# Kernel tuning notes

Measured on AMD Instinct MI355X. Metric: run time of the kernel, lower is better.

Reference implementation:

```python
import jax, jax.numpy as jnp
import numpy as np

G = 4            # group order (e.g., C4)
H = 16           # attention heads
DH = 64          # head dim
D = 1024         # token dim = H*DH = C*G
DI = 4096        # FFN inner dim
MAXREL = 32      # relative position clamp
EPS = 1e-5


def eq_ln(x):
    # Equivariant LayerNorm: (N, D) -> (N, G, D/G), LN over last dim, no affine
    N, Dt = x.shape
    xr = x.reshape(N, G, Dt // G)
    mu = jnp.mean(xr, axis=-1, keepdims=True)
    var = jnp.var(xr, axis=-1, keepdims=True)
    return ((xr - mu) * jax.lax.rsqrt(var + EPS)).reshape(N, Dt)


def ada_ln(x, temb, w, b):
    # AdaLN: scale/shift from SiLU(temb) -> Linear -> chunk
    n = eq_ln(x)
    ss = jax.nn.silu(temb) @ w.T + b                      # (N, 2D)
    scale, shift = jnp.split(ss, 2, axis=1)
    return n * (1.0 + scale) + shift


def attention(xq, xkv, wq, wk, wv, wo, bo, rel_table):
    # xq: (B,Tq,D), xkv: (B,Tk,D); rel_table: (H, 2*MAXREL+1) or None
    B, Tq, _ = xq.shape
    Tk = xkv.shape[1]
    q = (xq @ wq.T).reshape(B, Tq, H, DH)
    k = (xkv @ wk.T).reshape(B, Tk, H, DH)
    v = (xkv @ wv.T).reshape(B, Tk, H, DH)
    scores = jnp.einsum('bthd,bkhd->bhtk', q, k) * (DH ** -0.5)
    if rel_table is not None:
        rel_idx = jnp.clip(jnp.arange(Tq)[:, None] - jnp.arange(Tk)[None, :],
                           -MAXREL, MAXREL) + MAXREL      # (Tq, Tk)
        scores = scores + rel_table[:, rel_idx][None]     # (1,H,Tq,Tk)
    attn = jax.nn.softmax(scores, axis=-1)
    out = jnp.einsum('bhtk,bkhd->bthd', attn, v).reshape(B, Tq, H * DH)
    return out @ wo.T + bo


def setup_inputs() -> dict:
    key = jax.random.key(0)
    ks = jax.random.split(key, 24)
    s = 0.02
    B, T = 4, 1024
    inp = {
        'hidden_states': jax.random.normal(ks[0], (B, T, D), jnp.float32),
        'encoder_hidden_states': jax.random.normal(ks[1], (B, T, D), jnp.float32),
        'temb': jax.random.normal(ks[2], (B * T, D), jnp.float32),
        # AdaLN 1 / 2
        'w_ada1': jax.random.normal(ks[3], (2 * D, D), jnp.float32) * s,
        'b_ada1': jnp.zeros((2 * D,), jnp.float32),
        'w_ada2': jax.random.normal(ks[4], (2 * D, D), jnp.float32) * s,
        'b_ada2': jnp.zeros((2 * D,), jnp.float32),
        # self-attention (attention_bias=False, out_bias=True)
        'wq1': jax.random.normal(ks[5], (D, D), jnp.float32) * s,
        'wk1': jax.random.normal(ks[6], (D, D), jnp.float32) * s,
        'wv1': jax.random.normal(ks[7], (D, D), jnp.float32) * s,
        'wo1': jax.random.normal(ks[8], (D, D), jnp.float32) * s,
        'bo1': jnp.zeros((D,), jnp.float32),
        'rel_bias': jax.random.normal(ks[9], (H, 2 * MAXREL + 1), jnp.float32) * s,
        # cross-attention
        'wq2': jax.random.normal(ks[10], (D, D), jnp.float32) * s,
        'wk2': jax.random.normal(ks[11], (D, D), jnp.float32) * s,
        'wv2': jax.random.normal(ks[12], (D, D), jnp.float32) * s,
        'wo2': jax.random.normal(ks[13], (D, D), jnp.float32) * s,
        'bo2': jnp.zeros((D,), jnp.float32),
        # GEGLU FFN
        'w_ff1': jax.random.normal(ks[14], (2 * DI, D), jnp.float32) * s,
        'b_ff1': jnp.zeros((2 * DI,), jnp.float32),
        'w_ff2': jax.random.normal(ks[15], (D, DI), jnp.float32) * s,
        'b_ff2': jnp.zeros((D,), jnp.float32),
    }
    return inp


def reference(hidden_states, encoder_hidden_states, temb,
              w_ada1, b_ada1, w_ada2, b_ada2,
              wq1, wk1, wv1, wo1, bo1, rel_bias,
              wq2, wk2, wv2, wo2, bo2,
              w_ff1, b_ff1, w_ff2, b_ff2):
    B, T, Dm = hidden_states.shape
    x = hidden_states.reshape(B * T, Dm)
    # 1) AdaLN + self-attention with relative position bias + residual
    x1 = ada_ln(x, temb, w_ada1, b_ada1).reshape(B, T, Dm)
    x = x + attention(x1, x1, wq1, wk1, wv1, wo1, bo1, rel_bias).reshape(B * T, Dm)
    # 2) AdaLN + cross-attention + residual
    x2 = ada_ln(x, temb, w_ada2, b_ada2).reshape(B, T, Dm)
    x = x + attention(x2, encoder_hidden_states, wq2, wk2, wv2, wo2, bo2,
                      None).reshape(B * T, Dm)
    # 3) LayerNorm + GEGLU FFN + residual
    n3 = eq_ln(x)
    h12 = n3 @ w_ff1.T + b_ff1                            # (N, 2*DI)
    a, g = jnp.split(h12, 2, axis=-1)
    ff = (a * jax.nn.gelu(g, approximate=False)) @ w_ff2.T + b_ff2
    x = x + ff
    return x.reshape(B, T, Dm)
```

## Files before the change

kernel.cpp:

```cpp
#include <hip/hip_runtime.h>
#include <math.h>

typedef __attribute__((ext_vector_type(4))) float f32x4;
typedef __attribute__((ext_vector_type(8))) __bf16 bf16x8;

#define MFMA_BF16(a, b, c) __builtin_amdgcn_mfma_f32_16x16x32_bf16((a), (b), (c), 0, 0, 0)

static __device__ __forceinline__ unsigned short f2b(float f) {
  unsigned int u = __float_as_uint(f);
  return (unsigned short)((u + 0x7FFFu + ((u >> 16) & 1u)) >> 16);
}
static __device__ __forceinline__ float b2f(unsigned short h) {
  return __uint_as_float(((unsigned int)h) << 16);
}
static __device__ __forceinline__ unsigned short bcvt(float f) {
  __bf16 h = (__bf16)f;
  return __builtin_bit_cast(unsigned short, h);
}

static __device__ __forceinline__ void gll16(const void* g, void* l) {
  __builtin_amdgcn_global_load_lds((const __attribute__((address_space(1))) void*)g,
                                   (__attribute__((address_space(3))) void*)l, 16, 0, 0);
}

struct CvtArgs {
  const float* src[12];
  unsigned short* dst[12];
  int start[12];
};
__global__ __launch_bounds__(256) void f2b_multi(CvtArgs a) {
  const int bid = blockIdx.x;
  int s = 11;
#pragma unroll
  for (int i = 11; i >= 1; --i)
    if (bid < a.start[i]) s = i - 1;
  const size_t i4 = (size_t)(bid - a.start[s]) * 256 + threadIdx.x;
  const float4 v = *(const float4*)(a.src[s] + i4 * 4);
  ushort4 o;
  o.x = f2b(v.x); o.y = f2b(v.y); o.z = f2b(v.z); o.w = f2b(v.w);
  *(ushort4*)(a.dst[s] + i4 * 4) = o;
}

__global__ __launch_bounds__(256) void f2bperm_kernel(const float* __restrict__ src,
                                                      unsigned short* __restrict__ dst) {
  const int r = blockIdx.x;
  const int rr = r & 4095;
  const int dr = ((rr >> 4) << 5) | ((r >> 12) << 4) | (rr & 15);
  const int c = threadIdx.x * 4;
  const float4 v = *(const float4*)(src + (size_t)r * 1024 + c);
  ushort4 o;
  o.x = f2b(v.x); o.y = f2b(v.y); o.z = f2b(v.z); o.w = f2b(v.w);
  *(ushort4*)(dst + (size_t)dr * 1024 + c) = o;
}

__global__ __launch_bounds__(256) void silu_kernel(const float* __restrict__ src,
                                                   unsigned short* __restrict__ dst, int n) {
  const int i = (blockIdx.x * 256 + threadIdx.x) * 4;
  if (i >= n) return;
  const float4 v = *(const float4*)(src + i);
  ushort4 o;
  o.x = f2b(v.x / (1.f + expf(-v.x)));
  o.y = f2b(v.y / (1.f + expf(-v.y)));
  o.z = f2b(v.z / (1.f + expf(-v.z)));
  o.w = f2b(v.w / (1.f + expf(-v.w)));
  *(ushort4*)(dst + i) = o;
}

template <int ADA>
__global__ __launch_bounds__(256) void eqln_kernel(const float* __restrict__ x,
                                                   const unsigned short* __restrict__ ss,
                                                   unsigned short* __restrict__ outp) {
  const int n = blockIdx.x;
  const int tid = threadIdx.x;
  const int g = tid >> 6, lane = tid & 63;
  const size_t base = (size_t)n * 1024 + g * 256 + lane * 4;
  const float4 v = *(const float4*)(x + base);
  float s = v.x + v.y + v.z + v.w;
  float s2 = v.x * v.x + v.y * v.y + v.z * v.z + v.w * v.w;
#pragma unroll
  for (int m = 1; m < 64; m <<= 1) {
    s += __shfl_xor(s, m, 64);
    s2 += __shfl_xor(s2, m, 64);
  }
  const float mu = s * (1.f / 256.f);
  const float var = s2 * (1.f / 256.f) - mu * mu;
  const float rs = rsqrtf(var + 1e-5f);
  float o0 = (v.x - mu) * rs, o1 = (v.y - mu) * rs, o2 = (v.z - mu) * rs, o3 = (v.w - mu) * rs;
  if (ADA) {
    const size_t sb = (size_t)n * 4096 + g * 256 + lane * 4;
    const ushort4 scv = *(const ushort4*)(ss + sb);
    const ushort4 shv = *(const ushort4*)(ss + sb + 1024);
    o0 = o0 * (1.f + b2f(scv.x)) + b2f(shv.x);
    o1 = o1 * (1.f + b2f(scv.y)) + b2f(shv.y);
    o2 = o2 * (1.f + b2f(scv.z)) + b2f(shv.z);
    o3 = o3 * (1.f + b2f(scv.w)) + b2f(shv.w);
  }
  ushort4 ov;
  ov.x = f2b(o0); ov.y = f2b(o1); ov.z = f2b(o2); ov.w = f2b(o3);
  *(ushort4*)(outp + base) = ov;
}

__global__ __launch_bounds__(256) void vtrans_kernel(const unsigned short* __restrict__ v,
                                                     unsigned short* __restrict__ vt, int T,
                                                     int ld) {
  const int t0 = blockIdx.x * 64, h = blockIdx.y, b = blockIdx.z;
  __shared__ unsigned short tile[64][65];
  const int tid = threadIdx.x;
#pragma unroll
  for (int rr = 0; rr < 2; ++rr) {
    const int tok = rr * 32 + (tid >> 3);
    const int d8 = (tid & 7) * 8;
    const uint4 x = *(const uint4*)(v + (size_t)(b * T + t0 + tok) * ld + h * 64 + d8);
    const unsigned int* xs = (const unsigned int*)&x;
#pragma unroll
    for (int j = 0; j < 4; ++j) {
      tile[d8 + 2 * j][tok] = (unsigned short)(xs[j] & 0xffffu);
      tile[d8 + 2 * j + 1][tok] = (unsigned short)(xs[j] >> 16);
    }
  }
  __syncthreads();
#pragma unroll
  for (int rr = 0; rr < 2; ++rr) {
    const int d = rr * 32 + (tid >> 3);
    const int t8 = (tid & 7) * 8;
    uint4 ov;
    unsigned int* ou = (unsigned int*)&ov;
#pragma unroll
    for (int j = 0; j < 4; ++j)
      ou[j] = (unsigned int)tile[d][t8 + 2 * j] | ((unsigned int)tile[d][t8 + 2 * j + 1] << 16);
    *(uint4*)(vt + ((size_t)((b * 16 + h) * 64 + d)) * T + t0 + t8) = ov;
  }
}

template <int BM, int BIAS, int RES, int OUTMODE>
__global__ __launch_bounds__(256, 4) void gemm_nt(const unsigned short* __restrict__ A,
                                                  const unsigned short* __restrict__ Bw,
                                                  const float* __restrict__ bias,
                                                  const float* res, void* Cout,
                                                  int M, int N, int K) {
  constexpr int MB = BM / 32;
  __shared__ unsigned short As[BM * 64];
  __shared__ unsigned short Bs[128 * 64];
  const int m0 = blockIdx.x * BM, n0 = blockIdx.y * 128;
  const int tid = threadIdx.x, lane = tid & 63;
  const int wr = (tid >> 7) & 1, wc = (tid >> 6) & 1;
  const int lr = lane & 15, ls = lane >> 4;

  const f32x4 fz = {0.f, 0.f, 0.f, 0.f};
  f32x4 acc[MB][4];
#pragma unroll
  for (int m = 0; m < MB; ++m)
#pragma unroll
    for (int n = 0; n < 4; ++n) acc[m][n] = fz;

  for (int k0 = 0; k0 < K; k0 += 64) {
#pragma unroll
    for (int it = 0; it < BM / 32; ++it) {
      const int u = it * 256 + tid;
      const int row = u >> 3, gs = (u & 7) ^ (row & 7);
      gll16(A + (size_t)(m0 + row) * K + k0 + gs * 8, As + u * 8);
    }
#pragma unroll
    for (int it = 0; it < 4; ++it) {
      const int u = it * 256 + tid;
      const int row = u >> 3, gs = (u & 7) ^ (row & 7);
      gll16(Bw + (size_t)(n0 + row) * K + k0 + gs * 8, Bs + u * 8);
    }
    __syncthreads();
#pragma unroll
    for (int kk = 0; kk < 2; ++kk) {
      bf16x8 af[MB], bfr[4];
#pragma unroll
      for (int m = 0; m < MB; ++m) {
        const int row = wr * (BM / 2) + m * 16 + lr;
        const int slot = (kk * 4 + ls) ^ (row & 7);
        af[m] = *(const bf16x8*)(As + row * 64 + slot * 8);
      }
#pragma unroll
      for (int n = 0; n < 4; ++n) {
        const int col = wc * 64 + n * 16 + lr;
        const int slot = (kk * 4 + ls) ^ (col & 7);
        bfr[n] = *(const bf16x8*)(Bs + col * 64 + slot * 8);
      }
#pragma unroll
      for (int m = 0; m < MB; ++m)
#pragma unroll
        for (int n = 0; n < 4; ++n) acc[m][n] = MFMA_BF16(af[m], bfr[n], acc[m][n]);
    }
    __syncthreads();
  }

  if (OUTMODE == 2) {
    const int pn0 = n0 + wc * 64;
#pragma unroll
    for (int m = 0; m < MB; ++m) {
#pragma unroll
      for (int j = 0; j < 2; ++j) {
        const int ocol = (pn0 >> 1) + j * 16 + lr;
        const float ba = bias[ocol];
        const float bg = bias[(N >> 1) + ocol];
#pragma unroll
        for (int r = 0; r < 4; ++r) {
          const int row = m0 + wr * (BM / 2) + m * 16 + ls * 4 + r;
          const float a = acc[m][2 * j][r] + ba;
          const float g = acc[m][2 * j + 1][r] + bg;
          const float gl = 0.5f * g * (1.f + erff(g * 0.70710678118654752f));
          ((unsigned short*)Cout)[(size_t)row * (N >> 1) + ocol] = f2b(a * gl);
        }
      }
    }
    return;
  }
#pragma unroll
  for (int m = 0; m < MB; ++m) {
#pragma unroll
    for (int n = 0; n < 4; ++n) {
      const int col = n0 + wc * 64 + n * 16 + lr;
      float bv = 0.f;
      if (BIAS) bv = bias[col];
#pragma unroll
      for (int r = 0; r < 4; ++r) {
        const int row = m0 + wr * (BM / 2) + m * 16 + ls * 4 + r;
        float v = acc[m][n][r] + bv;
        if (RES) v += res[(size_t)row * N + col];
        if (OUTMODE == 1)
          ((unsigned short*)Cout)[(size_t)row * N + col] = f2b(v);
        else
          ((float*)Cout)[(size_t)row * N + col] = v;
      }
    }
  }
}

template <int RELB>
__global__ __launch_bounds__(256) void attn_kernel(const unsigned short* __restrict__ q,
                                                   const unsigned short* __restrict__ k,
                                                   const unsigned short* __restrict__ vt,
                                                   const float* __restrict__ rel,
                                                   unsigned short* __restrict__ outp,
                                                   int ldq, int ldk) {
  const int lin = blockIdx.x + (blockIdx.y << 4) + (blockIdx.z << 8);
  const int xcd = lin & 7, s = lin >> 3;
  const int g = (xcd << 3) + (s >> 4);
  const int qb = s & 15;
  const int h = g & 15, b = g >> 4;
  const int tid = threadIdx.x;
  const int wid = tid >> 6, lane = tid & 63;
  const int lr = lane & 15, ls = lane >> 4;
  const int q0 = (qb << 6) + (wid << 4);
  const float L2E = 1.44269504088896340736f;

  __shared__ unsigned short Ks[2][128 * 64];
  __shared__ unsigned short Vs[2][64 * 128];
  __shared__ unsigned short plds[4][16][64];
  __shared__ float tbl[66];

  if (RELB && tid < 65) tbl[tid] = rel[h * 65 + tid] * L2E;

  bf16x8 qa0, qa1;
  {
    const unsigned short* qp = q + (size_t)(b * 1024 + q0 + lr) * ldq + h * 64 + ls * 8;
    const bf16x8 t0 = *(const bf16x8*)qp;
    const bf16x8 t1 = *(const bf16x8*)(qp + 32);
    const float sc = 0.125f * L2E;
#pragma unroll
    for (int j = 0; j < 8; ++j) {
      qa0[j] = (__bf16)((float)t0[j] * sc);
      qa1[j] = (__bf16)((float)t1[j] * sc);
    }
  }
  bf16x8 ones;
#pragma unroll
  for (int j = 0; j < 8; ++j) ones[j] = (__bf16)1.0f;

  const f32x4 fz = {0.f, 0.f, 0.f, 0.f};
  f32x4 oacc[4];
#pragma unroll
  for (int d = 0; d < 4; ++d) oacc[d] = fz;
  f32x4 lacc = fz;

  const unsigned short* kbp = k + (size_t)(b * 1024) * ldk + h * 64;
  const unsigned short* vbp = vt + (size_t)((b * 16 + h) * 64) * 1024;

  auto stageK = [&](int buf, int kv0) {
#pragma unroll
    for (int it = 0; it < 4; ++it) {
      const int u = it * 256 + tid;
      const int row = u >> 3, gs = (u & 7) ^ (row & 7);
      gll16(kbp + (size_t)(kv0 + row) * ldk + gs * 8, Ks[buf] + u * 8);
    }
  };
  auto stageV = [&](int buf, int kv0) {
#pragma unroll
    for (int it = 0; it < 4; ++it) {
      const int u = it * 256 + tid;
      const int row = u >> 4;
      const int ch = u & 15;
      const int gs = (ch & 8) | ((ch & 7) ^ (row & 7));
      gll16(vbp + (size_t)row * 1024 + kv0 + gs * 8, Vs[buf] + u * 8);
    }
  };

  stageK(0, 0);
  stageV(0, 0);
  __syncthreads();

  for (int t = 0; t < 8; ++t) {
    const int kv0 = t << 7;
    if (t + 1 < 8) {
      stageV((t + 1) & 1, kv0 + 128);
      stageK((t + 1) & 1, kv0 + 128);
    }
    const unsigned short* kbuf = Ks[t & 1];
    const unsigned short* vbuf = Vs[t & 1];
#pragma unroll
    for (int sub = 0; sub < 2; ++sub) {
      const int kvs = kv0 + sub * 64;
      f32x4 sc4[4];
      __builtin_amdgcn_s_setprio(1);
#pragma unroll
      for (int nn = 0; nn < 4; ++nn) {
        const int row = sub * 64 + nn * 16 + lr;
        const int s0 = ls ^ (row & 7), s1 = (4 + ls) ^ (row & 7);
        const bf16x8 kb0 = *(const bf16x8*)(kbuf + row * 64 + s0 * 8);
        const bf16x8 kb1 = *(const bf16x8*)(kbuf + row * 64 + s1 * 8);
        f32x4 acc = fz;
        acc = MFMA_BF16(qa0, kb0, acc);
        acc = MFMA_BF16(qa1, kb1, acc);
        sc4[nn] = acc;
      }
      __builtin_amdgcn_s_setprio(0);
      float cb = 0.f;
      bool vary = false;
      if (RELB) {
        if (kvs + 95 <= q0) {
          cb = tbl[64];
        } else if (kvs >= q0 + 47) {
          cb = tbl[0];
        } else {
          vary = true;
        }
      }
      if (vary) {
        const int bd = q0 + ls * 4 - (kvs + lr);
#pragma unroll
        for (int nn = 0; nn < 4; ++nn)
#pragma unroll
          for (int r = 0; r < 4; ++r) {
            int dl = bd + r - nn * 16;
            dl = dl < -32 ? -32 : (dl > 32 ? 32 : dl);
            const float p = __builtin_amdgcn_exp2f(fminf(sc4[nn][r] + tbl[dl + 32], 60.f));
            const int qq = ls * 4 + r;
            const int colw = ((((nn << 1) + (lr >> 3)) ^ (qq & 7)) << 3) + (lr & 7);
            plds[wid][qq][colw] = bcvt(p);
          }
      } else {
#pragma unroll
        for (int nn = 0; nn < 4; ++nn)
#pragma unroll
          for (int r = 0; r < 4; ++r) {
            const float p = __builtin_amdgcn_exp2f(fminf(sc4[nn][r] + cb, 60.f));
            const int qq = ls * 4 + r;
            const int colw = ((((nn << 1) + (lr >> 3)) ^ (qq & 7)) << 3) + (lr & 7);
            plds[wid][qq][colw] = bcvt(p);
          }
      }
      asm volatile("" ::: "memory");
      const bf16x8 pa0 = *(const bf16x8*)&plds[wid][lr][((ls ^ (lr & 7)) << 3)];
      const bf16x8 pa1 = *(const bf16x8*)&plds[wid][lr][(((4 + ls) ^ (lr & 7)) << 3)];
      __builtin_amdgcn_s_setprio(1);
      lacc = MFMA_BF16(pa0, ones, lacc);
      lacc = MFMA_BF16(pa1, ones, lacc);
#pragma unroll
      for (int d = 0; d < 4; ++d) {
        const int rr = d * 16 + lr;
        const int c0 = sub * 8 + ls;
        const int c1 = c0 + 4;
        const int c0s = (c0 & 8) | ((c0 & 7) ^ (rr & 7));
        const int c1s = (c1 & 8) | ((c1 & 7) ^ (rr & 7));
        const bf16x8 vb0 = *(const bf16x8*)(vbuf + rr * 128 + c0s * 8);
        const bf16x8 vb1 = *(const bf16x8*)(vbuf + rr * 128 + c1s * 8);
        oacc[d] = MFMA_BF16(pa0, vb0, oacc[d]);
        oacc[d] = MFMA_BF16(pa1, vb1, oacc[d]);
      }
      __builtin_amdgcn_s_setprio(0);
    }
    __syncthreads();
  }

  float rinv[4];
#pragma unroll
  for (int r = 0; r < 4; ++r) rinv[r] = 1.0f / lacc[r];
#pragma unroll
  for (int d = 0; d < 4; ++d)
#pragma unroll
    for (int r = 0; r < 4; ++r) {
      const float v = oacc[d][r] * rinv[r];
      outp[(size_t)(b * 1024 + q0 + ls * 4 + r) * 1024 + h * 64 + d * 16 + lr] = bcvt(v);
    }
}

extern "C" void kernel_launch(void* const* d_in, const int* in_sizes, int n_in,
                              void* d_out, int out_size, void* d_ws, size_t ws_size,
                              hipStream_t stream) {
  (void)in_sizes; (void)n_in; (void)out_size; (void)ws_size;
  const float* hs = (const float*)d_in[0];
  const float* enc = (const float*)d_in[1];
  const float* temb = (const float*)d_in[2];
  const float* wada1 = (const float*)d_in[3];
  const float* bada1 = (const float*)d_in[4];
  const float* wada2 = (const float*)d_in[5];
  const float* bada2 = (const float*)d_in[6];
  const float* wq1 = (const float*)d_in[7];
  const float* wk1 = (const float*)d_in[8];
  const float* wv1 = (const float*)d_in[9];
  const float* wo1 = (const float*)d_in[10];
  const float* bo1 = (const float*)d_in[11];
  const float* rel = (const float*)d_in[12];
  const float* wq2 = (const float*)d_in[13];
  const float* wk2 = (const float*)d_in[14];
  const float* wv2 = (const float*)d_in[15];
  const float* wo2 = (const float*)d_in[16];
  const float* bo2 = (const float*)d_in[17];
  const float* wff1 = (const float*)d_in[18];
  const float* bff1 = (const float*)d_in[19];
  const float* wff2 = (const float*)d_in[20];
  const float* bff2 = (const float*)d_in[21];
  float* out = (float*)d_out;

  char* ws = (char*)d_ws;
  const size_t MB = 1024ull * 1024ull;
  unsigned short* wb_ada = (unsigned short*)(ws + 0 * MB);
  unsigned short* wb_q1 = (unsigned short*)(ws + 8 * MB);
  unsigned short* wb_k1 = (unsigned short*)(ws + 10 * MB);
  unsigned short* wb_v1 = (unsigned short*)(ws + 12 * MB);
  unsigned short* wb_o1 = (unsigned short*)(ws + 14 * MB);
  unsigned short* wb_q2 = (unsigned short*)(ws + 16 * MB);
  unsigned short* wb_k2 = (unsigned short*)(ws + 18 * MB);
  unsigned short* wb_v2 = (unsigned short*)(ws + 20 * MB);
  unsigned short* wb_o2 = (unsigned short*)(ws + 22 * MB);
  unsigned short* wb_ff1 = (unsigned short*)(ws + 24 * MB);
  unsigned short* wb_ff2 = (unsigned short*)(ws + 40 * MB);
  unsigned short* silu_t = (unsigned short*)(ws + 48 * MB);
  unsigned short* enc_b = (unsigned short*)(ws + 56 * MB);
  unsigned short* ssb = (unsigned short*)(ws + 64 * MB);
  unsigned short* ffin = (unsigned short*)(ws + 64 * MB);
  float* bias_cat = (float*)(ws + 96 * MB);
  unsigned short* x1b = (unsigned short*)(ws + 97 * MB);
  unsigned short* qkvb = (unsigned short*)(ws + 105 * MB);
  unsigned short* qb = (unsigned short*)(ws + 105 * MB);
  unsigned short* kvb = (unsigned short*)(ws + 113 * MB);
  unsigned short* vtb = (unsigned short*)(ws + 129 * MB);
  unsigned short* aob = (unsigned short*)(ws + 137 * MB);

  const int Nrow = 4096;

  {
    CvtArgs a;
    const float* srcs[12] = {wada1, wada2, wq1, wk1, wv1, wo1, wq2, wk2, wv2, wo2, wff2, enc};
    unsigned short* dsts[12] = {wb_ada, wb_ada + 2048 * 1024, wb_q1, wb_k1, wb_v1, wb_o1,
                                wb_q2, wb_k2, wb_v2, wb_o2, wb_ff2, enc_b};
    const int blks[12] = {2048, 2048, 1024, 1024, 1024, 1024, 1024, 1024, 1024, 1024, 4096, 4096};
    int acc = 0;
    for (int i = 0; i < 12; ++i) { a.src[i] = srcs[i]; a.dst[i] = dsts[i]; a.start[i] = acc; acc += blks[i]; }
    f2b_multi<<<acc, 256, 0, stream>>>(a);
  }
  (void)hipMemcpyAsync(bias_cat, bada1, 2048 * sizeof(float), hipMemcpyDeviceToDevice, stream);
  (void)hipMemcpyAsync(bias_cat + 2048, bada2, 2048 * sizeof(float), hipMemcpyDeviceToDevice, stream);
  f2bperm_kernel<<<8192, 256, 0, stream>>>(wff1, wb_ff1);
  silu_kernel<<<4096, 256, 0, stream>>>(temb, silu_t, 4096 * 1024);

  gemm_nt<128, 1, 0, 1><<<dim3(32, 32), 256, 0, stream>>>(silu_t, wb_ada, bias_cat, nullptr, ssb, Nrow, 4096, 1024);

  eqln_kernel<1><<<4096, 256, 0, stream>>>(hs, ssb, x1b);
  gemm_nt<128, 0, 0, 1><<<dim3(32, 24), 256, 0, stream>>>(x1b, wb_q1, nullptr, nullptr, qkvb, Nrow, 3072, 1024);
  vtrans_kernel<<<dim3(16, 16, 4), 256, 0, stream>>>(qkvb + 2048, vtb, 1024, 3072);
  attn_kernel<1><<<dim3(16, 16, 4), 256, 0, stream>>>(qkvb, qkvb + 1024, vtb, rel, aob, 3072, 3072);
  gemm_nt<64, 1, 1, 0><<<dim3(64, 8), 256, 0, stream>>>(aob, wb_o1, bo1, hs, out, Nrow, 1024, 1024);

  eqln_kernel<1><<<4096, 256, 0, stream>>>(out, ssb + 2048, x1b);
  gemm_nt<64, 0, 0, 1><<<dim3(64, 8), 256, 0, stream>>>(x1b, wb_q2, nullptr, nullptr, qb, Nrow, 1024, 1024);
  gemm_nt<128, 0, 0, 1><<<dim3(32, 16), 256, 0, stream>>>(enc_b, wb_k2, nullptr, nullptr, kvb, Nrow, 2048, 1024);
  vtrans_kernel<<<dim3(16, 16, 4), 256, 0, stream>>>(kvb + 1024, vtb, 1024, 2048);
  attn_kernel<0><<<dim3(16, 16, 4), 256, 0, stream>>>(qb, kvb, vtb, nullptr, aob, 1024, 2048);
  gemm_nt<64, 1, 1, 0><<<dim3(64, 8), 256, 0, stream>>>(aob, wb_o2, bo2, out, out, Nrow, 1024, 1024);

  eqln_kernel<0><<<4096, 256, 0, stream>>>(out, nullptr, x1b);
  gemm_nt<128, 1, 0, 2><<<dim3(32, 64), 256, 0, stream>>>(x1b, wb_ff1, bff1, nullptr, ffin, Nrow, 8192, 1024);
  gemm_nt<64, 1, 1, 0><<<dim3(64, 8), 256, 0, stream>>>(ffin, wb_ff2, bff2, out, out, Nrow, 1024, 4096);
}
```

Before: 428.3 us.

## Shrink attention KV tiles to single-buffered 64-row tiles to cut LDS use

The attention kernel drops its double-buffered 128-row K/V shared-memory tiles and uses one 64-row K and V tile per iteration. The next tile is loaded only after the current one is consumed. This cuts LDS from about 66KB to about 18KB, so more blocks can fit on each CU. In exchange, load/compute overlap inside a block is lost and there are twice as many iterations and barriers.

```diff
diff --git a/kernel.cpp b/kernel.cpp
--- a/kernel.cpp
+++ b/kernel.cpp
@@ -250,8 +250,8 @@
   const int q0 = (qb << 6) + (wid << 4);
   const float L2E = 1.44269504088896340736f;
 
-  __shared__ unsigned short Ks[2][128 * 64];
-  __shared__ unsigned short Vs[2][64 * 128];
+  __shared__ unsigned short Ks[64 * 64];
+  __shared__ unsigned short Vs[64 * 64];
   __shared__ unsigned short plds[4][16][64];
   __shared__ float tbl[66];
 
@@ -282,110 +282,101 @@
   const unsigned short* kbp = k + (size_t)(b * 1024) * ldk + h * 64;
   const unsigned short* vbp = vt + (size_t)((b * 16 + h) * 64) * 1024;
 
-  auto stageK = [&](int buf, int kv0) {
-#pragma unroll
-    for (int it = 0; it < 4; ++it) {
+  auto stageK = [&](int kv0) {
+#pragma unroll
+    for (int it = 0; it < 2; ++it) {
       const int u = it * 256 + tid;
       const int row = u >> 3, gs = (u & 7) ^ (row & 7);
-      gll16(kbp + (size_t)(kv0 + row) * ldk + gs * 8, Ks[buf] + u * 8);
+      gll16(kbp + (size_t)(kv0 + row) * ldk + gs * 8, Ks + u * 8);
     }
   };
-  auto stageV = [&](int buf, int kv0) {
-#pragma unroll
-    for (int it = 0; it < 4; ++it) {
+  auto stageV = [&](int kv0) {
+#pragma unroll
+    for (int it = 0; it < 2; ++it) {
       const int u = it * 256 + tid;
-      const int row = u >> 4;
-      const int ch = u & 15;
-      const int gs = (ch & 8) | ((ch & 7) ^ (row & 7));
-      gll16(vbp + (size_t)row * 1024 + kv0 + gs * 8, Vs[buf] + u * 8);
+      const int row = u >> 3, ch = u & 7;
+      const int gs = ch ^ (row & 7);
+      gll16(vbp + (size_t)row * 1024 + kv0 + gs * 8, Vs + u * 8);
     }
   };
 
-  stageK(0, 0);
-  stageV(0, 0);
-  __syncthreads();
-
-  for (int t = 0; t < 8; ++t) {
-    const int kv0 = t << 7;
-    if (t + 1 < 8) {
-      stageV((t + 1) & 1, kv0 + 128);
-      stageK((t + 1) & 1, kv0 + 128);
-    }
-    const unsigned short* kbuf = Ks[t & 1];
-    const unsigned short* vbuf = Vs[t & 1];
-#pragma unroll
-    for (int sub = 0; sub < 2; ++sub) {
-      const int kvs = kv0 + sub * 64;
-      f32x4 sc4[4];
-      __builtin_amdgcn_s_setprio(1);
-#pragma unroll
-      for (int nn = 0; nn < 4; ++nn) {
-        const int row = sub * 64 + nn * 16 + lr;
-        const int s0 = ls ^ (row & 7), s1 = (4 + ls) ^ (row & 7);
-        const bf16x8 kb0 = *(const bf16x8*)(kbuf + row * 64 + s0 * 8);
-        const bf16x8 kb1 = *(const bf16x8*)(kbuf + row * 64 + s1 * 8);
-        f32x4 acc = fz;
-        acc = MFMA_BF16(qa0, kb0, acc);
-        acc = MFMA_BF16(qa1, kb1, acc);
-        sc4[nn] = acc;
+  stageK(0);
+  stageV(0);
+
+  for (int t = 0; t < 16; ++t) {
+    const int kvs = t << 6;
+    __syncthreads();
+    f32x4 sc4[4];
+    __builtin_amdgcn_s_setprio(1);
+#pragma unroll
+    for (int nn = 0; nn < 4; ++nn) {
+      const int row = nn * 16 + lr;
+      const int s0 = ls ^ (row & 7), s1 = (4 + ls) ^ (row & 7);
+      const bf16x8 kb0 = *(const bf16x8*)(Ks + row * 64 + s0 * 8);
+      const bf16x8 kb1 = *(const bf16x8*)(Ks + row * 64 + s1 * 8);
+      f32x4 acc = fz;
+      acc = MFMA_BF16(qa0, kb0, acc);
+      acc = MFMA_BF16(qa1, kb1, acc);
+      sc4[nn] = acc;
+    }
+    __builtin_amdgcn_s_setprio(0);
+    float cb = 0.f;
+    bool vary = false;
+    if (RELB) {
+      if (kvs + 95 <= q0) {
+        cb = tbl[64];
+      } else if (kvs >= q0 + 47) {
+        cb = tbl[0];
+      } else {
+        vary = true;
       }
-      __builtin_amdgcn_s_setprio(0);
-      float cb = 0.f;
-      bool vary = false;
-      if (RELB) {
-        if (kvs + 95 <= q0) {
-          cb = tbl[64];
-        } else if (kvs >= q0 + 47) {
-          cb = tbl[0];
-        } else {
-          vary = true;
+    }
+    if (vary) {
+      const int bd = q0 + ls * 4 - (kvs + lr);
+#pragma unroll
+      for (int nn = 0; nn < 4; ++nn)
+#pragma unroll
+        for (int r = 0; r < 4; ++r) {
+          int dl = bd + r - nn * 16;
+          dl = dl < -32 ? -32 : (dl > 32 ? 32 : dl);
+          const float p = __builtin_amdgcn_exp2f(fminf(sc4[nn][r] + tbl[dl + 32], 60.f));
+          const int qq = ls * 4 + r;
+          const int colw = ((((nn << 1) + (lr >> 3)) ^ (qq & 7)) << 3) + (lr & 7);
+          plds[wid][qq][colw] = bcvt(p);
         }
-      }
-      if (vary) {
-        const int bd = q0 + ls * 4 - (kvs + lr);
-#pragma unroll
-        for (int nn = 0; nn < 4; ++nn)
-#pragma unroll
-          for (int r = 0; r < 4; ++r) {
-            int dl = bd + r - nn * 16;
-            dl = dl < -32 ? -32 : (dl > 32 ? 32 : dl);
-            const float p = __builtin_amdgcn_exp2f(fminf(sc4[nn][r] + tbl[dl + 32], 60.f));
-            const int qq = ls * 4 + r;
-            const int colw = ((((nn << 1) + (lr >> 3)) ^ (qq & 7)) << 3) + (lr & 7);
-            plds[wid][qq][colw] = bcvt(p);
-          }
-      } else {
-#pragma unroll
-        for (int nn = 0; nn < 4; ++nn)
-#pragma unroll
-          for (int r = 0; r < 4; ++r) {
-            const float p = __builtin_amdgcn_exp2f(fminf(sc4[nn][r] + cb, 60.f));
-            const int qq = ls * 4 + r;
-            const int colw = ((((nn << 1) + (lr >> 3)) ^ (qq & 7)) << 3) + (lr & 7);
-            plds[wid][qq][colw] = bcvt(p);
-          }
-      }
-      asm volatile("" ::: "memory");
-      const bf16x8 pa0 = *(const bf16x8*)&plds[wid][lr][((ls ^ (lr & 7)) << 3)];
-      const bf16x8 pa1 = *(const bf16x8*)&plds[wid][lr][(((4 + ls) ^ (lr & 7)) << 3)];
-      __builtin_amdgcn_s_setprio(1);
-      lacc = MFMA_BF16(pa0, ones, lacc);
-      lacc = MFMA_BF16(pa1, ones, lacc);
-#pragma unroll
-      for (int d = 0; d < 4; ++d) {
-        const int rr = d * 16 + lr;
-        const int c0 = sub * 8 + ls;
-        const int c1 = c0 + 4;
-        const int c0s = (c0 & 8) | ((c0 & 7) ^ (rr & 7));
-        const int c1s = (c1 & 8) | ((c1 & 7) ^ (rr & 7));
-        const bf16x8 vb0 = *(const bf16x8*)(vbuf + rr * 128 + c0s * 8);
-        const bf16x8 vb1 = *(const bf16x8*)(vbuf + rr * 128 + c1s * 8);
-        oacc[d] = MFMA_BF16(pa0, vb0, oacc[d]);
-        oacc[d] = MFMA_BF16(pa1, vb1, oacc[d]);
-      }
-      __builtin_amdgcn_s_setprio(0);
-    }
+    } else {
+#pragma unroll
+      for (int nn = 0; nn < 4; ++nn)
+#pragma unroll
+        for (int r = 0; r < 4; ++r) {
+          const float p = __builtin_amdgcn_exp2f(fminf(sc4[nn][r] + cb, 60.f));
+          const int qq = ls * 4 + r;
+          const int colw = ((((nn << 1) + (lr >> 3)) ^ (qq & 7)) << 3) + (lr & 7);
+          plds[wid][qq][colw] = bcvt(p);
+        }
+    }
+    asm volatile("" ::: "memory");
+    const bf16x8 pa0 = *(const bf16x8*)&plds[wid][lr][((ls ^ (lr & 7)) << 3)];
+    const bf16x8 pa1 = *(const bf16x8*)&plds[wid][lr][(((4 + ls) ^ (lr & 7)) << 3)];
+    __builtin_amdgcn_s_setprio(1);
+    lacc = MFMA_BF16(pa0, ones, lacc);
+    lacc = MFMA_BF16(pa1, ones, lacc);
+#pragma unroll
+    for (int d = 0; d < 4; ++d) {
+      const int rr = d * 16 + lr;
+      const int c0s = ls ^ (rr & 7);
+      const int c1s = (4 + ls) ^ (rr & 7);
+      const bf16x8 vb0 = *(const bf16x8*)(Vs + rr * 64 + c0s * 8);
+      const bf16x8 vb1 = *(const bf16x8*)(Vs + rr * 64 + c1s * 8);
+      oacc[d] = MFMA_BF16(pa0, vb0, oacc[d]);
+      oacc[d] = MFMA_BF16(pa1, vb1, oacc[d]);
+    }
+    __builtin_amdgcn_s_setprio(0);
     __syncthreads();
+    if (t + 1 < 16) {
+      stageK(kvs + 64);
+      stageV(kvs + 64);
+    }
   }
 
   float rinv[4];
```

After: 438.2 us. 2.3% more time.
